# Performance work log

Hardware: AMD Instinct MI355X
Metric: run time of the kernel (lower is better)

Reference implementation:

```python
import jax, jax.numpy as jnp
import numpy as np
import math

H = 12  # num heads
EPS = 1e-5


def layer_norm(x, g, b):
    xf = x.astype(jnp.float32)
    mu = jnp.mean(xf, axis=-1, keepdims=True)
    var = jnp.var(xf, axis=-1, keepdims=True)
    return ((xf - mu) * jax.lax.rsqrt(var + EPS) * g + b).astype(x.dtype)


def setup_inputs() -> dict:
    key = jax.random.key(0)
    ks = jax.random.split(key, 8)
    C, M = 768, 3072
    s = 0.02
    inp = {
        "x": jax.random.normal(ks[0], (128, 197, C), dtype=jnp.float32),
        # linear weights stored as [in, out] (y = x @ W + b)
        "Wq": jax.random.normal(ks[1], (C, C), dtype=jnp.float32) * s,
        "bq": jnp.zeros((C,), jnp.float32),
        "Wk": jax.random.normal(ks[2], (C, C), dtype=jnp.float32) * s,
        "bk": jnp.zeros((C,), jnp.float32),
        "Wv": jax.random.normal(ks[3], (C, C), dtype=jnp.float32) * s,
        "bv": jnp.zeros((C,), jnp.float32),
        "Wo": jax.random.normal(ks[4], (C, C), dtype=jnp.float32) * s,
        "bo": jnp.zeros((C,), jnp.float32),
        "W1": jax.random.normal(ks[5], (C, M), dtype=jnp.float32) * s,
        "b1": jnp.zeros((M,), jnp.float32),
        "W2": jax.random.normal(ks[6], (M, C), dtype=jnp.float32) * s,
        "b2": jnp.zeros((C,), jnp.float32),
        "g1": jnp.ones((C,), jnp.float32),
        "beta1": jnp.zeros((C,), jnp.float32),
        "g2": jnp.ones((C,), jnp.float32),
        "beta2": jnp.zeros((C,), jnp.float32),
    }
    return inp


def attention(xn, Wq, bq, Wk, bk, Wv, bv, Wo, bo):
    N, L, C = xn.shape
    Cqk = C // H
    q = (xn @ Wq + bq).reshape(N, L, H, Cqk)
    k = (xn @ Wk + bk).reshape(N, L, H, Cqk)
    v = (xn @ Wv + bv).reshape(N, L, H, Cqk)
    scale = 1.0 / math.sqrt(Cqk)
    aff = jnp.einsum('nqhc,nkhc->nqkh', q * scale, k)  # [N, Lq, Lk, H]
    aff = jax.nn.softmax(aff, axis=-2)                  # softmax over key axis
    mix = jnp.einsum('nqlh,nlhc->nqhc', aff, v)
    return mix.reshape(N, L, C) @ Wo + bo


def reference(x, Wq, bq, Wk, bk, Wv, bv, Wo, bo, W1, b1, W2, b2, g1, beta1, g2, beta2):
    x = x + attention(layer_norm(x, g1, beta1), Wq, bq, Wk, bk, Wv, bv, Wo, bo)
    h = layer_norm(x, g2, beta2) @ W1 + b1
    h = h * jax.nn.sigmoid(1.702 * h)  # QuickGELU
    return x + h @ W2 + b2
```

## Files before the change

kernel.cpp:

```cpp
#include <hip/hip_runtime.h>
#include <hip/hip_bf16.h>

typedef __bf16 bf16_t;
typedef __bf16 bf16x8 __attribute__((ext_vector_type(8)));
typedef float f32x4 __attribute__((ext_vector_type(4)));

#define T_TOK 25216
#define C_DIM 768
#define NH 12
#define LSEQ 197

__device__ __forceinline__ void gload_lds16(const bf16_t* g, bf16_t* l) {
  __builtin_amdgcn_global_load_lds(
      (const __attribute__((address_space(1))) unsigned int*)g,
      (__attribute__((address_space(3))) unsigned int*)l, 16, 0, 0);
}

template <int N>
__device__ __forceinline__ void vm_wait() {
  asm volatile("s_waitcnt vmcnt(%0)" ::"n"(N) : "memory");
}
__device__ __forceinline__ void block_bar() {
  __builtin_amdgcn_sched_barrier(0);
  asm volatile("" ::: "memory");
  __builtin_amdgcn_s_barrier();
  __builtin_amdgcn_sched_barrier(0);
}

__global__ void wtrans_k(const float* __restrict__ W, bf16_t* __restrict__ Wt,
                         int K, int N) {
  __shared__ float tile[32][33];
  const int tx = threadIdx.x, ty = threadIdx.y;
  const int bx = blockIdx.x, by = blockIdx.y;
#pragma unroll
  for (int i = ty; i < 32; i += 8)
    tile[i][tx] = W[(long)(by * 32 + i) * N + bx * 32 + tx];
  __syncthreads();
#pragma unroll
  for (int i = ty; i < 32; i += 8)
    Wt[(long)(bx * 32 + i) * K + by * 32 + tx] = (bf16_t)tile[tx][i];
}

__global__ void cat3_k(const float* __restrict__ a, const float* __restrict__ b,
                       const float* __restrict__ c, float* __restrict__ o) {
  int i = blockIdx.x * 256 + threadIdx.x;
  if (i < 2304) o[i] = i < 768 ? a[i] : (i < 1536 ? b[i - 768] : c[i - 1536]);
}

__global__ __launch_bounds__(256) void ln_k(const float* __restrict__ x,
                                            const float* __restrict__ g,
                                            const float* __restrict__ b,
                                            bf16_t* __restrict__ o) {
  const int lane = threadIdx.x & 63;
  const long row = (long)blockIdx.x * 4 + (threadIdx.x >> 6);
  const float* xr = x + row * C_DIM;
  float4 v[3];
  float s = 0.f, sq = 0.f;
#pragma unroll
  for (int i = 0; i < 3; ++i) {
    v[i] = *(const float4*)&xr[i * 256 + lane * 4];
    s += v[i].x + v[i].y + v[i].z + v[i].w;
    sq += v[i].x * v[i].x + v[i].y * v[i].y + v[i].z * v[i].z + v[i].w * v[i].w;
  }
#pragma unroll
  for (int off = 32; off; off >>= 1) {
    s += __shfl_xor(s, off);
    sq += __shfl_xor(sq, off);
  }
  const float mu = s * (1.f / 768.f);
  const float rstd = rsqrtf(sq * (1.f / 768.f) - mu * mu + 1e-5f);
  bf16_t* orow = o + row * C_DIM;
#pragma unroll
  for (int i = 0; i < 3; ++i) {
    const int c = i * 256 + lane * 4;
    const float4 gg = *(const float4*)&g[c];
    const float4 bb = *(const float4*)&b[c];
    bf16_t t4[4];
    t4[0] = (bf16_t)((v[i].x - mu) * rstd * gg.x + bb.x);
    t4[1] = (bf16_t)((v[i].y - mu) * rstd * gg.y + bb.y);
    t4[2] = (bf16_t)((v[i].z - mu) * rstd * gg.z + bb.z);
    t4[3] = (bf16_t)((v[i].w - mu) * rstd * gg.w + bb.w);
    __builtin_memcpy(&orow[c], t4, 8);
  }
}

template <int EPI, int BM, int BN>
__global__ __launch_bounds__(256) void gemm_bt(
    const bf16_t* __restrict__ A, const bf16_t* __restrict__ Bt,
    const float* __restrict__ bias, const float* __restrict__ res,
    void* __restrict__ outp, int K, int N) {
  constexpr int BK = 32;
  constexpr int MACC = BM / 32;
  constexpr int NACC = BN / 32;
  constexpr int ACW = BM / 64;
  constexpr int BCW = BN / 64;
  constexpr int NLOADS = ACW + BCW;
  __shared__ __align__(16) bf16_t lA[2][BM * BK];
  __shared__ __align__(16) bf16_t lB[2][BN * BK];
  const int tid = threadIdx.x;
  const int wave = tid >> 6, lane = tid & 63;
  const int fr = lane & 15, fq = lane >> 4;

  const int gx = gridDim.x;
  const int nwg = gridDim.x * gridDim.y;
  int bid = blockIdx.y * gx + blockIdx.x;
  {
    const int q = nwg >> 3, r = nwg & 7;
    const int xcd = bid & 7, idx = bid >> 3;
    bid = (xcd < r ? xcd * (q + 1) : r * (q + 1) + (xcd - r) * q) + idx;
  }
  const int bx = bid % gx, by = bid / gx;

  const long rowBase = (long)by * BM;
  const long colBase = (long)bx * BN;
  const int wr = (wave >> 1) * (BM / 2), wc = (wave & 1) * (BN / 2);

  f32x4 acc[MACC][NACC];
#pragma unroll
  for (int m = 0; m < MACC; ++m)
#pragma unroll
    for (int n = 0; n < NACC; ++n) acc[m][n] = (f32x4){0.f, 0.f, 0.f, 0.f};

  const int srow = lane >> 2;
  const int scol = (((lane & 3) ^ ((srow >> 1) & 3))) * 8;
  const int rdsw = (fq ^ ((fr >> 1) & 3)) * 8;

  const bf16_t* aP[ACW];
  const bf16_t* bP[BCW];
#pragma unroll
  for (int c = 0; c < ACW; ++c)
    aP[c] = A + (rowBase + 16 * (wave * ACW + c) + srow) * (long)K + scol;
#pragma unroll
  for (int c = 0; c < BCW; ++c)
    bP[c] = Bt + (colBase + 16 * (wave * BCW + c) + srow) * (long)K + scol;

  auto stage0 = [&](int koff) {
#pragma unroll
    for (int c = 0; c < ACW; ++c)
      gload_lds16(aP[c] + koff, &lA[0][(wave * ACW + c) * 512]);
#pragma unroll
    for (int c = 0; c < BCW; ++c)
      gload_lds16(bP[c] + koff, &lB[0][(wave * BCW + c) * 512]);
  };
  auto stage1 = [&](int koff) {
#pragma unroll
    for (int c = 0; c < ACW; ++c)
      gload_lds16(aP[c] + koff, &lA[1][(wave * ACW + c) * 512]);
#pragma unroll
    for (int c = 0; c < BCW; ++c)
      gload_lds16(bP[c] + koff, &lB[1][(wave * BCW + c) * 512]);
  };
  auto compute0 = [&]() {
    bf16x8 af[MACC], bfr[NACC];
#pragma unroll
    for (int m = 0; m < MACC; ++m)
      af[m] = *(const bf16x8*)&lA[0][(wr + m * 16 + fr) * BK + rdsw];
#pragma unroll
    for (int n = 0; n < NACC; ++n)
      bfr[n] = *(const bf16x8*)&lB[0][(wc + n * 16 + fr) * BK + rdsw];
#pragma unroll
    for (int m = 0; m < MACC; ++m)
#pragma unroll
      for (int n = 0; n < NACC; ++n)
        acc[m][n] = __builtin_amdgcn_mfma_f32_16x16x32_bf16(af[m], bfr[n],
                                                            acc[m][n], 0, 0, 0);
  };
  auto compute1 = [&]() {
    bf16x8 af[MACC], bfr[NACC];
#pragma unroll
    for (int m = 0; m < MACC; ++m)
      af[m] = *(const bf16x8*)&lA[1][(wr + m * 16 + fr) * BK + rdsw];
#pragma unroll
    for (int n = 0; n < NACC; ++n)
      bfr[n] = *(const bf16x8*)&lB[1][(wc + n * 16 + fr) * BK + rdsw];
#pragma unroll
    for (int m = 0; m < MACC; ++m)
#pragma unroll
      for (int n = 0; n < NACC; ++n)
        acc[m][n] = __builtin_amdgcn_mfma_f32_16x16x32_bf16(af[m], bfr[n],
                                                            acc[m][n], 0, 0, 0);
  };

  const int kT = K >> 5;
  stage0(0);
  int kt = 0;
  for (; kt + 2 < kT; kt += 2) {
    stage1((kt + 1) * BK);
    vm_wait<NLOADS>();
    block_bar();
    compute0();
    block_bar();
    stage0((kt + 2) * BK);
    vm_wait<NLOADS>();
    block_bar();
    compute1();
    block_bar();
  }
  stage1((kt + 1) * BK);
  vm_wait<NLOADS>();
  block_bar();
  compute0();
  vm_wait<0>();
  block_bar();
  compute1();

#pragma unroll
  for (int m = 0; m < MACC; ++m) {
    const long row0 = rowBase + wr + m * 16 + fq * 4;
#pragma unroll
    for (int n = 0; n < NACC; ++n) {
      const long col = colBase + wc + n * 16 + fr;
      const float bb = bias[col];
#pragma unroll
      for (int r = 0; r < 4; ++r) {
        const long idx = (row0 + r) * N + col;
        float v = acc[m][n][r] + bb;
        if (EPI == 0) {
          ((bf16_t*)outp)[idx] = (bf16_t)v;
        } else if (EPI == 1) {
          ((float*)outp)[idx] = v + res[idx];
        } else {
          v = v / (1.f + __expf(-1.702f * v));
          ((bf16_t*)outp)[idx] = (bf16_t)v;
        }
      }
    }
  }
}

__global__ __launch_bounds__(256) void attn_k(const bf16_t* __restrict__ qkv,
                                              bf16_t* __restrict__ mix) {
  constexpr int KR = 72;
  constexpr int VR = 232;
  __shared__ __align__(16) bf16_t smem[208 * KR + 64 * VR + 64 * VR];
  bf16_t* lK = smem;
  bf16_t* lVt = smem + 208 * KR;
  bf16_t* lP = lVt + 64 * VR;

  const int tid = threadIdx.x;
  const int wave = tid >> 6, lane = tid & 63;
  const int fr = lane & 15, fq = lane >> 4;
  const int nh = blockIdx.x;
  const int n = nh / NH, h = nh % NH;
  const long t0 = (long)n * LSEQ;
  const long qs = 2304;

  {
    int4 z = {0, 0, 0, 0};
    int4* p = (int4*)smem;
    const int tot = (208 * KR + 2 * 64 * VR) * 2 / 16;
    for (int i = tid; i < tot; i += 256) p[i] = z;
  }
  __syncthreads();

  for (int it = tid; it < 197 * 8; it += 256) {
    int r = it >> 3, cg = it & 7;
    int4 v = *(const int4*)(qkv + (t0 + r) * qs + 768 + h * 64 + cg * 8);
    *(int4*)&lK[r * KR + cg * 8] = v;
  }
  for (int it = tid; it < 197 * 8; it += 256) {
    int r = it >> 3, cg = it & 7;
    int4 v = *(const int4*)(qkv + (t0 + r) * qs + 1536 + h * 64 + cg * 8);
    const bf16_t* pv = (const bf16_t*)&v;
#pragma unroll
    for (int j = 0; j < 8; ++j) lVt[(cg * 8 + j) * VR + r] = pv[j];
  }
  __syncthreads();

  bf16_t* lPw = lP + wave * 16 * VR;

  for (int fi = 0; fi < 4; ++fi) {
    const int f = wave + fi * 4;
    if (f >= 13) break;
    const int qrow = f * 16 + fr;
    const long tq = t0 + (qrow < LSEQ ? qrow : LSEQ - 1);
    const bf16_t* qp = qkv + tq * qs + h * 64;
    bf16x8 a0 = *(const bf16x8*)(qp + fq * 8);
    bf16x8 a1 = *(const bf16x8*)(qp + 32 + fq * 8);

    f32x4 s[13];
#pragma unroll
    for (int j = 0; j < 13; ++j) s[j] = (f32x4){0.f, 0.f, 0.f, 0.f};
#pragma unroll
    for (int j = 0; j < 13; ++j) {
      bf16x8 b0 = *(const bf16x8*)&lK[(j * 16 + fr) * KR + fq * 8];
      s[j] = __builtin_amdgcn_mfma_f32_16x16x32_bf16(a0, b0, s[j], 0, 0, 0);
      bf16x8 b1 = *(const bf16x8*)&lK[(j * 16 + fr) * KR + 32 + fq * 8];
      s[j] = __builtin_amdgcn_mfma_f32_16x16x32_bf16(a1, b1, s[j], 0, 0, 0);
    }
    float mx[4] = {-3e38f, -3e38f, -3e38f, -3e38f};
#pragma unroll
    for (int j = 0; j < 13; ++j) {
      const bool valid = (j * 16 + fr) < LSEQ;
#pragma unroll
      for (int r = 0; r < 4; ++r) {
        float v = s[j][r] * 0.125f;
        v = valid ? v : -3e38f;
        s[j][r] = v;
        mx[r] = fmaxf(mx[r], v);
      }
    }
#pragma unroll
    for (int r = 0; r < 4; ++r) {
      mx[r] = fmaxf(mx[r], __shfl_xor(mx[r], 1));
      mx[r] = fmaxf(mx[r], __shfl_xor(mx[r], 2));
      mx[r] = fmaxf(mx[r], __shfl_xor(mx[r], 4));
      mx[r] = fmaxf(mx[r], __shfl_xor(mx[r], 8));
    }
    float sm[4] = {0.f, 0.f, 0.f, 0.f};
#pragma unroll
    for (int j = 0; j < 13; ++j)
#pragma unroll
      for (int r = 0; r < 4; ++r) {
        float e = __expf(s[j][r] - mx[r]);
        s[j][r] = e;
        sm[r] += e;
      }
#pragma unroll
    for (int r = 0; r < 4; ++r) {
      sm[r] += __shfl_xor(sm[r], 1);
      sm[r] += __shfl_xor(sm[r], 2);
      sm[r] += __shfl_xor(sm[r], 4);
      sm[r] += __shfl_xor(sm[r], 8);
      sm[r] = 1.f / sm[r];
    }
#pragma unroll
    for (int j = 0; j < 13; ++j)
#pragma unroll
      for (int r = 0; r < 4; ++r)
        lPw[(fq * 4 + r) * VR + j * 16 + fr] = (bf16_t)(s[j][r] * sm[r]);
    asm volatile("s_waitcnt lgkmcnt(0)" ::: "memory");

    f32x4 o4[4];
#pragma unroll
    for (int c = 0; c < 4; ++c) o4[c] = (f32x4){0.f, 0.f, 0.f, 0.f};
#pragma unroll
    for (int kc = 0; kc < 7; ++kc) {
      bf16x8 pa = *(const bf16x8*)&lPw[fr * VR + kc * 32 + fq * 8];
#pragma unroll
      for (int c = 0; c < 4; ++c) {
        bf16x8 bv = *(const bf16x8*)&lVt[(c * 16 + fr) * VR + kc * 32 + fq * 8];
        o4[c] = __builtin_amdgcn_mfma_f32_16x16x32_bf16(pa, bv, o4[c], 0, 0, 0);
      }
    }
#pragma unroll
    for (int c = 0; c < 4; ++c)
#pragma unroll
      for (int r = 0; r < 4; ++r) {
        const int q = f * 16 + fq * 4 + r;
        if (q < LSEQ)
          mix[(t0 + q) * C_DIM + h * 64 + c * 16 + fr] = (bf16_t)o4[c][r];
      }
  }
}

extern "C" void kernel_launch(void* const* d_in, const int* in_sizes, int n_in,
                              void* d_out, int out_size, void* d_ws,
                              size_t ws_size, hipStream_t stream) {
  const float* x = (const float*)d_in[0];
  const float* Wq = (const float*)d_in[1];
  const float* bq = (const float*)d_in[2];
  const float* Wk = (const float*)d_in[3];
  const float* bk = (const float*)d_in[4];
  const float* Wv = (const float*)d_in[5];
  const float* bv = (const float*)d_in[6];
  const float* Wo = (const float*)d_in[7];
  const float* bo = (const float*)d_in[8];
  const float* W1 = (const float*)d_in[9];
  const float* b1 = (const float*)d_in[10];
  const float* W2 = (const float*)d_in[11];
  const float* b2 = (const float*)d_in[12];
  const float* g1 = (const float*)d_in[13];
  const float* be1 = (const float*)d_in[14];
  const float* g2 = (const float*)d_in[15];
  const float* be2 = (const float*)d_in[16];

  char* ws = (char*)d_ws;
  size_t off = 0;
  auto alloc = [&](size_t bytes) {
    char* p = ws + off;
    off += (bytes + 255) & ~(size_t)255;
    return p;
  };
  bf16_t* xn = (bf16_t*)alloc((size_t)T_TOK * 768 * 2);
  char* qm = alloc((size_t)T_TOK * 3072 * 2);
  bf16_t* qkv = (bf16_t*)qm;
  bf16_t* mixb = (bf16_t*)(qm + (size_t)T_TOK * 2304 * 2);
  bf16_t* h = (bf16_t*)qm;
  bf16_t* Wqkvt = (bf16_t*)alloc((size_t)2304 * 768 * 2);
  bf16_t* Wot = (bf16_t*)alloc((size_t)768 * 768 * 2);
  bf16_t* W1t = (bf16_t*)alloc((size_t)3072 * 768 * 2);
  bf16_t* W2t = (bf16_t*)alloc((size_t)768 * 3072 * 2);
  float* bqkv = (float*)alloc(2304 * 4);
  float* x2 = (float*)d_out;

  dim3 tb(32, 8);
  wtrans_k<<<dim3(24, 24), tb, 0, stream>>>(Wq, Wqkvt, 768, 768);
  wtrans_k<<<dim3(24, 24), tb, 0, stream>>>(Wk, Wqkvt + 768 * 768, 768, 768);
  wtrans_k<<<dim3(24, 24), tb, 0, stream>>>(Wv, Wqkvt + 2 * 768 * 768, 768, 768);
  wtrans_k<<<dim3(24, 24), tb, 0, stream>>>(Wo, Wot, 768, 768);
  wtrans_k<<<dim3(96, 24), tb, 0, stream>>>(W1, W1t, 768, 3072);
  wtrans_k<<<dim3(24, 96), tb, 0, stream>>>(W2, W2t, 3072, 768);
  cat3_k<<<9, 256, 0, stream>>>(bq, bk, bv, bqkv);

  ln_k<<<T_TOK / 4, 256, 0, stream>>>(x, g1, be1, xn);
  gemm_bt<0, 128, 128><<<dim3(2304 / 128, T_TOK / 128), 256, 0, stream>>>(
      xn, Wqkvt, bqkv, nullptr, qkv, 768, 2304);
  attn_k<<<128 * NH, 256, 0, stream>>>(qkv, mixb);
  gemm_bt<1, 128, 128><<<dim3(768 / 128, T_TOK / 128), 256, 0, stream>>>(
      mixb, Wot, bo, x, x2, 768, 768);
  ln_k<<<T_TOK / 4, 256, 0, stream>>>(x2, g2, be2, xn);
  gemm_bt<2, 128, 128><<<dim3(3072 / 128, T_TOK / 128), 256, 0, stream>>>(
      xn, W1t, b1, nullptr, h, 768, 3072);
  gemm_bt<1, 128, 128><<<dim3(768 / 128, T_TOK / 128), 256, 0, stream>>>(
      h, W2t, b2, x2, (float*)d_out, 3072, 768);
}
```

Before: 785.6 us.

## Load B fragments directly to registers and deepen K tile to 64

The GEMM now stages only the A tile through LDS, with a new XOR swizzle for a 64-wide K tile. B fragments are loaded straight from global memory into registers with double buffering, and each stage's K depth doubles from 32 to 64. This halves the barrier count per K and removes the LDS traffic for B, but each wave now loads its own B fragments with uncoalesced 16-byte reads and holds more registers, which may lower occupancy.

```diff
diff --git a/kernel.cpp b/kernel.cpp
--- a/kernel.cpp
+++ b/kernel.cpp
@@ -89,14 +89,11 @@
     const bf16_t* __restrict__ A, const bf16_t* __restrict__ Bt,
     const float* __restrict__ bias, const float* __restrict__ res,
     void* __restrict__ outp, int K, int N) {
-  constexpr int BK = 32;
   constexpr int MACC = BM / 32;
   constexpr int NACC = BN / 32;
-  constexpr int ACW = BM / 64;
-  constexpr int BCW = BN / 64;
-  constexpr int NLOADS = ACW + BCW;
-  __shared__ __align__(16) bf16_t lA[2][BM * BK];
-  __shared__ __align__(16) bf16_t lB[2][BN * BK];
+  constexpr int ACW = BM / 32;
+  constexpr int NLOADS = ACW + NACC * 2;
+  __shared__ __align__(16) bf16_t lA[2][BM * 64];
   const int tid = threadIdx.x;
   const int wave = tid >> 6, lane = tid & 63;
   const int fr = lane & 15, fq = lane >> 4;
@@ -121,88 +118,81 @@
 #pragma unroll
     for (int n = 0; n < NACC; ++n) acc[m][n] = (f32x4){0.f, 0.f, 0.f, 0.f};
 
-  const int srow = lane >> 2;
-  const int scol = (((lane & 3) ^ ((srow >> 1) & 3))) * 8;
-  const int rdsw = (fq ^ ((fr >> 1) & 3)) * 8;
+  const int srow = lane >> 3;
+  const int scol = (((lane & 7) ^ srow)) * 8;
 
   const bf16_t* aP[ACW];
-  const bf16_t* bP[BCW];
 #pragma unroll
   for (int c = 0; c < ACW; ++c)
-    aP[c] = A + (rowBase + 16 * (wave * ACW + c) + srow) * (long)K + scol;
-#pragma unroll
-  for (int c = 0; c < BCW; ++c)
-    bP[c] = Bt + (colBase + 16 * (wave * BCW + c) + srow) * (long)K + scol;
-
-  auto stage0 = [&](int koff) {
+    aP[c] = A + (rowBase + 8 * (wave * ACW + c) + srow) * (long)K + scol;
+  const bf16_t* bP[NACC];
+#pragma unroll
+  for (int n = 0; n < NACC; ++n)
+    bP[n] = Bt + (colBase + wc + n * 16 + fr) * (long)K + fq * 8;
+
+  bf16x8 bX[NACC][2], bY[NACC][2];
+
+  auto stageA0 = [&](int koff) {
 #pragma unroll
     for (int c = 0; c < ACW; ++c)
       gload_lds16(aP[c] + koff, &lA[0][(wave * ACW + c) * 512]);
-#pragma unroll
-    for (int c = 0; c < BCW; ++c)
-      gload_lds16(bP[c] + koff, &lB[0][(wave * BCW + c) * 512]);
   };
-  auto stage1 = [&](int koff) {
+  auto stageA1 = [&](int koff) {
 #pragma unroll
     for (int c = 0; c < ACW; ++c)
       gload_lds16(aP[c] + koff, &lA[1][(wave * ACW + c) * 512]);
-#pragma unroll
-    for (int c = 0; c < BCW; ++c)
-      gload_lds16(bP[c] + koff, &lB[1][(wave * BCW + c) * 512]);
   };
-  auto compute0 = [&]() {
-    bf16x8 af[MACC], bfr[NACC];
-#pragma unroll
-    for (int m = 0; m < MACC; ++m)
-      af[m] = *(const bf16x8*)&lA[0][(wr + m * 16 + fr) * BK + rdsw];
+  auto loadB = [&](bf16x8 (&dst)[NACC][2], int koff) {
 #pragma unroll
     for (int n = 0; n < NACC; ++n)
-      bfr[n] = *(const bf16x8*)&lB[0][(wc + n * 16 + fr) * BK + rdsw];
-#pragma unroll
-    for (int m = 0; m < MACC; ++m)
-#pragma unroll
-      for (int n = 0; n < NACC; ++n)
-        acc[m][n] = __builtin_amdgcn_mfma_f32_16x16x32_bf16(af[m], bfr[n],
-                                                            acc[m][n], 0, 0, 0);
+#pragma unroll
+      for (int kf = 0; kf < 2; ++kf)
+        dst[n][kf] = *(const bf16x8*)(bP[n] + koff + kf * 32);
   };
-  auto compute1 = [&]() {
-    bf16x8 af[MACC], bfr[NACC];
-#pragma unroll
-    for (int m = 0; m < MACC; ++m)
-      af[m] = *(const bf16x8*)&lA[1][(wr + m * 16 + fr) * BK + rdsw];
-#pragma unroll
-    for (int n = 0; n < NACC; ++n)
-      bfr[n] = *(const bf16x8*)&lB[1][(wc + n * 16 + fr) * BK + rdsw];
-#pragma unroll
-    for (int m = 0; m < MACC; ++m)
-#pragma unroll
-      for (int n = 0; n < NACC; ++n)
-        acc[m][n] = __builtin_amdgcn_mfma_f32_16x16x32_bf16(af[m], bfr[n],
-                                                            acc[m][n], 0, 0, 0);
+  auto compute = [&](const bf16_t* buf, const bf16x8 (&bv)[NACC][2]) {
+#pragma unroll
+    for (int kf = 0; kf < 2; ++kf) {
+      bf16x8 af[MACC];
+#pragma unroll
+      for (int m = 0; m < MACC; ++m)
+        af[m] =
+            *(const bf16x8*)&buf[(wr + m * 16 + fr) * 64 +
+                                 (((kf * 4 + fq) ^ (fr & 7)) * 8)];
+#pragma unroll
+      for (int m = 0; m < MACC; ++m)
+#pragma unroll
+        for (int n = 0; n < NACC; ++n)
+          acc[m][n] = __builtin_amdgcn_mfma_f32_16x16x32_bf16(af[m], bv[n][kf],
+                                                              acc[m][n], 0, 0, 0);
+    }
   };
 
-  const int kT = K >> 5;
-  stage0(0);
+  const int kT = K >> 6;
+  stageA0(0);
+  loadB(bX, 0);
   int kt = 0;
   for (; kt + 2 < kT; kt += 2) {
-    stage1((kt + 1) * BK);
+    stageA1((kt + 1) * 64);
+    loadB(bY, (kt + 1) * 64);
     vm_wait<NLOADS>();
     block_bar();
-    compute0();
+    compute(&lA[0][0], bX);
     block_bar();
-    stage0((kt + 2) * BK);
+    stageA0((kt + 2) * 64);
+    loadB(bX, (kt + 2) * 64);
     vm_wait<NLOADS>();
     block_bar();
-    compute1();
+    compute(&lA[1][0], bY);
     block_bar();
   }
-  stage1((kt + 1) * BK);
+  stageA1((kt + 1) * 64);
+  loadB(bY, (kt + 1) * 64);
   vm_wait<NLOADS>();
   block_bar();
-  compute0();
+  compute(&lA[0][0], bX);
   vm_wait<0>();
   block_bar();
-  compute1();
+  compute(&lA[1][0], bY);
 
 #pragma unroll
   for (int m = 0; m < MACC; ++m) {
```

After: 1.019 ms. 1.3x slower.
